# Performance work log

Hardware: AMD Instinct MI355X
Metric: run time of the kernel (lower is better)

## Reference

```python
import jax, jax.numpy as jnp
import numpy as np

A, B_HI = 0.0, 1.0          # support interval
NUM_GRIDS = 256
DEGREE = 2
KNOTS = (0.33, 0.66)
NUM_BASIS = DEGREE + 1 + len(KNOTS)  # 5


def spline_basis(d):
    # Truncated power basis: [1, d, d^2, relu(d-k1)^2, relu(d-k2)^2] -> [B, NUM_BASIS]
    cols = [jnp.ones_like(d)]
    for p in range(1, DEGREE + 1):
        cols.append(d ** p)
    for k in KNOTS:
        cols.append(jax.nn.relu(d - k) ** DEGREE)
    return jnp.stack(cols, axis=1)


def setup_inputs() -> dict:
    key = jax.random.key(0)
    k1, k2, k3, k4 = jax.random.split(key, 4)
    B, IN = 65536, 128
    OUT = NUM_GRIDS + 1
    d = jax.random.uniform(k1, (B,), dtype=jnp.float32)          # treatment in [0,1]
    z = jax.random.normal(k2, (B, IN), dtype=jnp.float32)        # encoder features
    weight = jax.random.uniform(k3, (IN, OUT, NUM_BASIS), dtype=jnp.float32)  # torch.rand init
    bias = jax.random.uniform(k4, (OUT, NUM_BASIS), dtype=jnp.float32)
    return {"d": d, "z": z, "weight": weight, "bias": bias}


def reference(d, z, weight, bias):
    basis = spline_basis(d)  # [B, NB]
    # einsum('ab,bcd->acd') then sum over basis dim, fused into one contraction
    out = jnp.einsum('bi,ion,bn->bo', z, weight, basis) + basis @ bias.T  # [B, OUT]
    # linear interpolation params (faithful to get_linear_interpolation_params,
    # including tmp = (d - a) * (b - a))
    tmp = (d - A) * (B_HI - A)
    g = tmp * NUM_GRIDS
    lower = jnp.clip(jnp.floor(g), 0, NUM_GRIDS - 1)
    upper = jnp.clip(jnp.ceil(g), 0, NUM_GRIDS - 1)
    dist = g - lower
    li = lower.astype(jnp.int32)
    ui = upper.astype(jnp.int32)
    ix = jnp.arange(out.shape[0])
    lb = out[ix, li]
    ub = out[ix, ui]
    prob = lb + (ub - lb) * dist
    in_support = (d >= A) & (d <= B_HI)
    return prob * in_support.astype(prob.dtype)
```

## Files before the change

### kernel.cpp

```cpp
#include <hip/hip_runtime.h>
#include <math.h>


constexpr int IN_F = 128;
constexpr int OUTC = 257;
constexpr int NB   = 5;

__global__ __launch_bounds__(256) void transpose_w_kernel(
    const float* __restrict__ w, float* __restrict__ wT)
{
    int idx = blockIdx.x * blockDim.x + threadIdx.x;
    constexpr int TOT = OUTC * NB * IN_F;
    if (idx >= TOT) return;
    int i    = idx & (IN_F - 1);
    int rest = idx >> 7;
    int n    = rest % NB;
    int o    = rest / NB;
    wT[idx] = w[(size_t)i * (OUTC * NB) + o * NB + n];
}

template<bool TR>
__global__ __launch_bounds__(256) void vcd_main(
    const float* __restrict__ dtr, const float* __restrict__ z,
    const float* __restrict__ w,   const float* __restrict__ bias,
    float* __restrict__ out, int B)
{
    int t   = blockIdx.x * blockDim.x + threadIdx.x;
    int row = t >> 4;
    int s   = threadIdx.x & 15;
    if (row >= B) return;

    float dv = dtr[row];

    float b1 = dv, b2 = dv * dv;
    float r1 = fmaxf(dv - 0.33f, 0.0f);
    float r2 = fmaxf(dv - 0.66f, 0.0f);
    float b3 = r1 * r1, b4 = r2 * r2;

    float g     = dv * 256.0f;
    float lower = fminf(fmaxf(floorf(g), 0.0f), 255.0f);
    float dist  = g - lower;
    int   li = (int)lower;
    int   ui = min(li + 1, 255);

    const float4* zv = reinterpret_cast<const float4*>(z + (size_t)row * IN_F + s * 8);
    float4 z0 = zv[0], z1 = zv[1];
    float zz[8] = {z0.x, z0.y, z0.z, z0.w, z1.x, z1.y, z1.z, z1.w};

    float accl = 0.0f, accu = 0.0f;

    if constexpr (TR) {
        const float* wl = w + (size_t)li * (NB * IN_F) + s * 8;
        const float* wu = w + (size_t)ui * (NB * IN_F) + s * 8;
        #pragma unroll
        for (int n = 0; n < NB; ++n) {
            float bn = (n == 0) ? 1.0f : (n == 1) ? b1 : (n == 2) ? b2 : (n == 3) ? b3 : b4;
            float4 l0 = reinterpret_cast<const float4*>(wl + n * IN_F)[0];
            float4 l1 = reinterpret_cast<const float4*>(wl + n * IN_F)[1];
            float4 u0 = reinterpret_cast<const float4*>(wu + n * IN_F)[0];
            float4 u1 = reinterpret_cast<const float4*>(wu + n * IN_F)[1];
            float dl = zz[0]*l0.x + zz[1]*l0.y + zz[2]*l0.z + zz[3]*l0.w
                     + zz[4]*l1.x + zz[5]*l1.y + zz[6]*l1.z + zz[7]*l1.w;
            float du = zz[0]*u0.x + zz[1]*u0.y + zz[2]*u0.z + zz[3]*u0.w
                     + zz[4]*u1.x + zz[5]*u1.y + zz[6]*u1.z + zz[7]*u1.w;
            accl = fmaf(bn, dl, accl);
            accu = fmaf(bn, du, accu);
        }
    } else {
        #pragma unroll
        for (int k = 0; k < 8; ++k) {
            const float* wp  = w + (size_t)(s * 8 + k) * (OUTC * NB);
            const float* wlp = wp + li * NB;
            const float* wup = wp + ui * NB;
            float wsl = wlp[0] + b1*wlp[1] + b2*wlp[2] + b3*wlp[3] + b4*wlp[4];
            float wsu = wup[0] + b1*wup[1] + b2*wup[2] + b3*wup[3] + b4*wup[4];
            accl = fmaf(zz[k], wsl, accl);
            accu = fmaf(zz[k], wsu, accu);
        }
    }

    float comb = fmaf(dist, accu - accl, accl);
    #pragma unroll
    for (int m = 1; m < 16; m <<= 1)
        comb += __shfl_xor(comb, m, 64);

    if (s == 0) {
        const float* blp = bias + li * NB;
        const float* bup = bias + ui * NB;
        float bl = blp[0] + b1*blp[1] + b2*blp[2] + b3*blp[3] + b4*blp[4];
        float bu = bup[0] + b1*bup[1] + b2*bup[2] + b3*bup[3] + b4*bup[4];
        float prob = comb + fmaf(dist, bu - bl, bl);
        bool sup = (dv >= 0.0f) && (dv <= 1.0f);
        out[row] = sup ? prob : 0.0f;
    }
}

extern "C" void kernel_launch(void* const* d_in, const int* in_sizes, int n_in,
                              void* d_out, int out_size, void* d_ws, size_t ws_size,
                              hipStream_t stream) {
    const float* d_d = (const float*)d_in[0];
    const float* d_z = (const float*)d_in[1];
    const float* d_w = (const float*)d_in[2];
    const float* d_b = (const float*)d_in[3];
    float* out = (float*)d_out;
    int B = in_sizes[0];

    constexpr size_t WT_BYTES = (size_t)OUTC * NB * IN_F * sizeof(float);
    int main_blocks = (B * 16 + 255) / 256;

    if (ws_size >= WT_BYTES) {
        float* wT = (float*)d_ws;
        constexpr int TOT = OUTC * NB * IN_F;
        transpose_w_kernel<<<(TOT + 255) / 256, 256, 0, stream>>>(d_w, wT);
        vcd_main<true><<<main_blocks, 256, 0, stream>>>(d_d, d_z, wT, d_b, out, B);
    } else {
        vcd_main<false><<<main_blocks, 256, 0, stream>>>(d_d, d_z, d_w, d_b, out, B);
    }
}
```

Measured before the change: 103.3 us.

## Bucket rows by grid cell and stage cell weights in LDS

Rows are bucketed by their lower grid index using atomic counters into a per-cell order list. A per-cell kernel then loads the two relevant weight slices and biases into shared memory once and processes all rows of that cell, replacing scattered per-row global weight gathers. Rows that overflow a bucket's capacity fall back to a serial per-thread dot product in the scatter kernel. The change adds an extra launch, atomics and an indirect z gather, and block counts are fixed at cells times split regardless of how many rows each cell holds.

```diff
diff --git a/kernel.cpp b/kernel.cpp
--- a/kernel.cpp
+++ b/kernel.cpp
@@ -2,95 +2,184 @@
 #include <math.h>
 
 
-constexpr int IN_F = 128;
-constexpr int OUTC = 257;
-constexpr int NB   = 5;
-
-__global__ __launch_bounds__(256) void transpose_w_kernel(
-    const float* __restrict__ w, float* __restrict__ wT)
-{
-    int idx = blockIdx.x * blockDim.x + threadIdx.x;
+constexpr int IN_F  = 128;
+constexpr int OUTC  = 257;
+constexpr int NB    = 5;
+constexpr int CELLS = 256;
+constexpr int CAP   = 1024;
+constexpr int SPLIT = 8;
+
+constexpr size_t ORDER_OFF = 4096;
+constexpr size_t WT_OFF    = ORDER_OFF + (size_t)CELLS * CAP * 4;
+constexpr size_t WS_NEED   = WT_OFF + (size_t)OUTC * NB * IN_F * 4;
+
+__global__ __launch_bounds__(256) void init_kernel(
+    const float* __restrict__ w, float* __restrict__ wT, int* __restrict__ cursor)
+{
+    int idx = blockIdx.x * 256 + threadIdx.x;
+    if (idx < CELLS) cursor[idx] = 0;
     constexpr int TOT = OUTC * NB * IN_F;
-    if (idx >= TOT) return;
-    int i    = idx & (IN_F - 1);
-    int rest = idx >> 7;
-    int n    = rest % NB;
-    int o    = rest / NB;
-    wT[idx] = w[(size_t)i * (OUTC * NB) + o * NB + n];
-}
-
-template<bool TR>
-__global__ __launch_bounds__(256) void vcd_main(
+    if (idx < TOT) {
+        int i    = idx & (IN_F - 1);
+        int rest = idx >> 7;
+        int n    = rest % NB;
+        int o    = rest / NB;
+        wT[idx] = w[(size_t)i * (OUTC * NB) + o * NB + n];
+    }
+}
+
+__global__ __launch_bounds__(256) void scatter_kernel(
+    const float* __restrict__ dtr, const float* __restrict__ z,
+    const float* __restrict__ wT,  const float* __restrict__ bias,
+    int* __restrict__ cursor, int* __restrict__ order,
+    float* __restrict__ out, int B)
+{
+    int row = blockIdx.x * 256 + threadIdx.x;
+    if (row >= B) return;
+    float dv = dtr[row];
+    float g  = dv * 256.0f;
+    int li   = (int)fminf(fmaxf(floorf(g), 0.0f), 255.0f);
+    int slot = atomicAdd(&cursor[li], 1);
+    if (slot < CAP) { order[li * CAP + slot] = row; return; }
+
+    int   ui   = min(li + 1, 255);
+    float dist = g - (float)li;
+    float b1 = dv, b2 = dv * dv;
+    float r1 = fmaxf(dv - 0.33f, 0.0f), r2 = fmaxf(dv - 0.66f, 0.0f);
+    float bas[NB] = {1.0f, b1, b2, r1 * r1, r2 * r2};
+    const float* wl = wT + (size_t)li * (NB * IN_F);
+    const float* wu = wT + (size_t)ui * (NB * IN_F);
+    const float* zr = z + (size_t)row * IN_F;
+    float accl = 0.0f, accu = 0.0f;
+    for (int n = 0; n < NB; ++n) {
+        float sl = 0.0f, su = 0.0f;
+        for (int i = 0; i < IN_F; ++i) {
+            sl = fmaf(zr[i], wl[n * IN_F + i], sl);
+            su = fmaf(zr[i], wu[n * IN_F + i], su);
+        }
+        accl = fmaf(bas[n], sl, accl);
+        accu = fmaf(bas[n], su, accu);
+    }
+    float bl = 0.0f, bu = 0.0f;
+    for (int n = 0; n < NB; ++n) {
+        bl = fmaf(bas[n], bias[li * NB + n], bl);
+        bu = fmaf(bas[n], bias[ui * NB + n], bu);
+    }
+    float lb = accl + bl, ub = accu + bu;
+    float prob = lb + (ub - lb) * dist;
+    bool  sup  = (dv >= 0.0f) && (dv <= 1.0f);
+    out[row] = sup ? prob : 0.0f;
+}
+
+__global__ __launch_bounds__(256) void main_kernel(
+    const float* __restrict__ dtr, const float* __restrict__ z,
+    const float* __restrict__ wT,  const float* __restrict__ bias,
+    const int* __restrict__ cursor, const int* __restrict__ order,
+    float* __restrict__ out)
+{
+    __shared__ float lds[2 * NB * IN_F + 2 * NB + 6];
+    int c = blockIdx.x / SPLIT;
+    int s = blockIdx.x % SPLIT;
+    int u = min(c + 1, 255);
+    int tid = threadIdx.x;
+
+    const float4* wl4 = reinterpret_cast<const float4*>(wT + (size_t)c * (NB * IN_F));
+    const float4* wu4 = reinterpret_cast<const float4*>(wT + (size_t)u * (NB * IN_F));
+    float4* l4 = reinterpret_cast<float4*>(lds);
+    for (int k = tid; k < 320; k += 256)
+        l4[k] = (k < 160) ? wl4[k] : wu4[k - 160];
+    if (tid < NB)            lds[1280 + tid] = bias[c * NB + tid];
+    else if (tid < 2 * NB)   lds[1280 + tid] = bias[u * NB + tid - NB];
+    __syncthreads();
+
+    int cnt  = min(cursor[c], CAP);
+    int grp  = tid >> 4;
+    int lane = tid & 15;
+
+    for (int j = s * 16 + grp; j < cnt; j += SPLIT * 16) {
+        int   row = order[c * CAP + j];
+        float dv  = dtr[row];
+        float b1 = dv, b2 = dv * dv;
+        float r1 = fmaxf(dv - 0.33f, 0.0f), r2 = fmaxf(dv - 0.66f, 0.0f);
+        float b3 = r1 * r1, b4 = r2 * r2;
+        float dist = dv * 256.0f - (float)c;
+
+        const float4* zv = reinterpret_cast<const float4*>(z + (size_t)row * IN_F + lane * 8);
+        float4 z0 = zv[0], z1 = zv[1];
+
+        float accl = 0.0f, accu = 0.0f;
+        #pragma unroll
+        for (int n = 0; n < NB; ++n) {
+            float bn = (n == 0) ? 1.0f : (n == 1) ? b1 : (n == 2) ? b2 : (n == 3) ? b3 : b4;
+            const float4* ln4 = reinterpret_cast<const float4*>(lds + n * IN_F);
+            const float4* un4 = reinterpret_cast<const float4*>(lds + NB * IN_F + n * IN_F);
+            float4 l0 = ln4[lane * 2], l1 = ln4[lane * 2 + 1];
+            float4 u0 = un4[lane * 2], u1 = un4[lane * 2 + 1];
+            float dl = z0.x*l0.x + z0.y*l0.y + z0.z*l0.z + z0.w*l0.w
+                     + z1.x*l1.x + z1.y*l1.y + z1.z*l1.z + z1.w*l1.w;
+            float du = z0.x*u0.x + z0.y*u0.y + z0.z*u0.z + z0.w*u0.w
+                     + z1.x*u1.x + z1.y*u1.y + z1.z*u1.z + z1.w*u1.w;
+            accl = fmaf(bn, dl, accl);
+            accu = fmaf(bn, du, accu);
+        }
+
+        float comb = fmaf(dist, accu - accl, accl);
+        #pragma unroll
+        for (int m = 1; m < 16; m <<= 1)
+            comb += __shfl_xor(comb, m, 64);
+
+        if (lane == 0) {
+            float bl = lds[1280] + b1*lds[1281] + b2*lds[1282] + b3*lds[1283] + b4*lds[1284];
+            float bu = lds[1285] + b1*lds[1286] + b2*lds[1287] + b3*lds[1288] + b4*lds[1289];
+            float prob = comb + fmaf(dist, bu - bl, bl);
+            bool  sup  = (dv >= 0.0f) && (dv <= 1.0f);
+            out[row] = sup ? prob : 0.0f;
+        }
+    }
+}
+
+__global__ __launch_bounds__(256) void direct_kernel(
     const float* __restrict__ dtr, const float* __restrict__ z,
     const float* __restrict__ w,   const float* __restrict__ bias,
     float* __restrict__ out, int B)
 {
     int t   = blockIdx.x * blockDim.x + threadIdx.x;
     int row = t >> 4;
-    int s   = threadIdx.x & 15;
+    int lane = threadIdx.x & 15;
     if (row >= B) return;
-
     float dv = dtr[row];
-
     float b1 = dv, b2 = dv * dv;
-    float r1 = fmaxf(dv - 0.33f, 0.0f);
-    float r2 = fmaxf(dv - 0.66f, 0.0f);
+    float r1 = fmaxf(dv - 0.33f, 0.0f), r2 = fmaxf(dv - 0.66f, 0.0f);
     float b3 = r1 * r1, b4 = r2 * r2;
-
-    float g     = dv * 256.0f;
+    float g = dv * 256.0f;
     float lower = fminf(fmaxf(floorf(g), 0.0f), 255.0f);
-    float dist  = g - lower;
-    int   li = (int)lower;
-    int   ui = min(li + 1, 255);
-
-    const float4* zv = reinterpret_cast<const float4*>(z + (size_t)row * IN_F + s * 8);
+    float dist = g - lower;
+    int li = (int)lower, ui = min(li + 1, 255);
+    const float4* zv = reinterpret_cast<const float4*>(z + (size_t)row * IN_F + lane * 8);
     float4 z0 = zv[0], z1 = zv[1];
     float zz[8] = {z0.x, z0.y, z0.z, z0.w, z1.x, z1.y, z1.z, z1.w};
-
     float accl = 0.0f, accu = 0.0f;
-
-    if constexpr (TR) {
-        const float* wl = w + (size_t)li * (NB * IN_F) + s * 8;
-        const float* wu = w + (size_t)ui * (NB * IN_F) + s * 8;
-        #pragma unroll
-        for (int n = 0; n < NB; ++n) {
-            float bn = (n == 0) ? 1.0f : (n == 1) ? b1 : (n == 2) ? b2 : (n == 3) ? b3 : b4;
-            float4 l0 = reinterpret_cast<const float4*>(wl + n * IN_F)[0];
-            float4 l1 = reinterpret_cast<const float4*>(wl + n * IN_F)[1];
-            float4 u0 = reinterpret_cast<const float4*>(wu + n * IN_F)[0];
-            float4 u1 = reinterpret_cast<const float4*>(wu + n * IN_F)[1];
-            float dl = zz[0]*l0.x + zz[1]*l0.y + zz[2]*l0.z + zz[3]*l0.w
-                     + zz[4]*l1.x + zz[5]*l1.y + zz[6]*l1.z + zz[7]*l1.w;
-            float du = zz[0]*u0.x + zz[1]*u0.y + zz[2]*u0.z + zz[3]*u0.w
-                     + zz[4]*u1.x + zz[5]*u1.y + zz[6]*u1.z + zz[7]*u1.w;
-            accl = fmaf(bn, dl, accl);
-            accu = fmaf(bn, du, accu);
-        }
-    } else {
-        #pragma unroll
-        for (int k = 0; k < 8; ++k) {
-            const float* wp  = w + (size_t)(s * 8 + k) * (OUTC * NB);
-            const float* wlp = wp + li * NB;
-            const float* wup = wp + ui * NB;
-            float wsl = wlp[0] + b1*wlp[1] + b2*wlp[2] + b3*wlp[3] + b4*wlp[4];
-            float wsu = wup[0] + b1*wup[1] + b2*wup[2] + b3*wup[3] + b4*wup[4];
-            accl = fmaf(zz[k], wsl, accl);
-            accu = fmaf(zz[k], wsu, accu);
-        }
-    }
-
+    #pragma unroll
+    for (int k = 0; k < 8; ++k) {
+        const float* wp  = w + (size_t)(lane * 8 + k) * (OUTC * NB);
+        const float* wlp = wp + li * NB;
+        const float* wup = wp + ui * NB;
+        float wsl = wlp[0] + b1*wlp[1] + b2*wlp[2] + b3*wlp[3] + b4*wlp[4];
+        float wsu = wup[0] + b1*wup[1] + b2*wup[2] + b3*wup[3] + b4*wup[4];
+        accl = fmaf(zz[k], wsl, accl);
+        accu = fmaf(zz[k], wsu, accu);
+    }
     float comb = fmaf(dist, accu - accl, accl);
     #pragma unroll
     for (int m = 1; m < 16; m <<= 1)
         comb += __shfl_xor(comb, m, 64);
-
-    if (s == 0) {
+    if (lane == 0) {
         const float* blp = bias + li * NB;
         const float* bup = bias + ui * NB;
         float bl = blp[0] + b1*blp[1] + b2*blp[2] + b3*blp[3] + b4*blp[4];
         float bu = bup[0] + b1*bup[1] + b2*bup[2] + b3*bup[3] + b4*bup[4];
         float prob = comb + fmaf(dist, bu - bl, bl);
-        bool sup = (dv >= 0.0f) && (dv <= 1.0f);
+        bool  sup  = (dv >= 0.0f) && (dv <= 1.0f);
         out[row] = sup ? prob : 0.0f;
     }
 }
@@ -105,15 +194,17 @@
     float* out = (float*)d_out;
     int B = in_sizes[0];
 
-    constexpr size_t WT_BYTES = (size_t)OUTC * NB * IN_F * sizeof(float);
-    int main_blocks = (B * 16 + 255) / 256;
-
-    if (ws_size >= WT_BYTES) {
-        float* wT = (float*)d_ws;
-        constexpr int TOT = OUTC * NB * IN_F;
-        transpose_w_kernel<<<(TOT + 255) / 256, 256, 0, stream>>>(d_w, wT);
-        vcd_main<true><<<main_blocks, 256, 0, stream>>>(d_d, d_z, wT, d_b, out, B);
-    } else {
-        vcd_main<false><<<main_blocks, 256, 0, stream>>>(d_d, d_z, d_w, d_b, out, B);
-    }
-}
+    if (ws_size < WS_NEED) {
+        direct_kernel<<<(B * 16 + 255) / 256, 256, 0, stream>>>(d_d, d_z, d_w, d_b, out, B);
+        return;
+    }
+
+    int*   cursor = (int*)d_ws;
+    int*   order  = (int*)((char*)d_ws + ORDER_OFF);
+    float* wT     = (float*)((char*)d_ws + WT_OFF);
+
+    constexpr int TOT = OUTC * NB * IN_F;
+    init_kernel<<<(TOT + 255) / 256, 256, 0, stream>>>(d_w, wT, cursor);
+    scatter_kernel<<<(B + 255) / 256, 256, 0, stream>>>(d_d, d_z, wT, d_b, cursor, order, out, B);
+    main_kernel<<<CELLS * SPLIT, 256, 0, stream>>>(d_d, d_z, wT, d_b, cursor, order, out);
+}
```

After: 121.8 us. 1.18x slower.

## Precompute per-interval quadratic coefficients folding knot terms into polynomial basis

Applied to the files above, without the earlier changes.

Replaces the weight transpose with a coefficient kernel that expands the truncated-power basis into plain quadratic coefficients per grid cell, with two extra sub-intervals for the cells containing the knots. Each row then loads 6 coefficient vectors instead of 10 weight vectors and evaluates the lower and upper quadratics by Horner's rule. The aim is to cut weight traffic and FMAs per row in the main kernel. The knot-cell selection relies on the float comparison against 0.33 and 0.66 matching the relu branch, which could introduce small rounding differences.

```diff
diff --git a/kernel.cpp b/kernel.cpp
--- a/kernel.cpp
+++ b/kernel.cpp
@@ -4,93 +4,142 @@
 
 constexpr int IN_F = 128;
 constexpr int OUTC = 257;
-constexpr int NB   = 5;
+constexpr int NSUB = 258;
+constexpr size_t A_FLOATS  = (size_t)NSUB * 6 * IN_F;
+constexpr size_t BQ_OFF_F  = A_FLOATS;
+constexpr size_t WS_NEED   = (A_FLOATS + NSUB * 6) * sizeof(float);
 
-__global__ __launch_bounds__(256) void transpose_w_kernel(
-    const float* __restrict__ w, float* __restrict__ wT)
+__global__ __launch_bounds__(256) void coeff_kernel(
+    const float* __restrict__ w, const float* __restrict__ bias,
+    float* __restrict__ A, float* __restrict__ Bq)
 {
-    int idx = blockIdx.x * blockDim.x + threadIdx.x;
-    constexpr int TOT = OUTC * NB * IN_F;
-    if (idx >= TOT) return;
-    int i    = idx & (IN_F - 1);
-    int rest = idx >> 7;
-    int n    = rest % NB;
-    int o    = rest / NB;
-    wT[idx] = w[(size_t)i * (OUTC * NB) + o * NB + n];
+    int t = blockIdx.x * 256 + threadIdx.x;
+    if (t >= NSUB * IN_F) return;
+    int i   = t & (IN_F - 1);
+    int idx = t >> 7;
+    int c   = (idx < 256) ? idx : (idx == 256 ? 84 : 168);
+    int u   = min(c + 1, 255);
+    float s1 = ((c >= 85) || (idx == 256)) ? 1.0f : 0.0f;
+    float s2 = ((c >= 169) || (idx == 257)) ? 1.0f : 0.0f;
+    const float k1 = 0.33f, k2 = 0.66f;
+
+    const float* wl = w + (size_t)i * (OUTC * 5) + c * 5;
+    const float* wu = w + (size_t)i * (OUTC * 5) + u * 5;
+    float q0l = wl[0] + s1 * k1 * k1 * wl[3] + s2 * k2 * k2 * wl[4];
+    float q1l = wl[1] - 2.0f * (s1 * k1 * wl[3] + s2 * k2 * wl[4]);
+    float q2l = wl[2] + s1 * wl[3] + s2 * wl[4];
+    float q0u = wu[0] + s1 * k1 * k1 * wu[3] + s2 * k2 * k2 * wu[4];
+    float q1u = wu[1] - 2.0f * (s1 * k1 * wu[3] + s2 * k2 * wu[4]);
+    float q2u = wu[2] + s1 * wu[3] + s2 * wu[4];
+
+    float* Ai = A + (size_t)idx * (6 * IN_F);
+    Ai[0 * IN_F + i] = q0l;  Ai[1 * IN_F + i] = q1l;  Ai[2 * IN_F + i] = q2l;
+    Ai[3 * IN_F + i] = q0u;  Ai[4 * IN_F + i] = q1u;  Ai[5 * IN_F + i] = q2u;
+
+    if (i == 0) {
+        const float* bl = bias + c * 5;
+        const float* bu = bias + u * 5;
+        float* bq = Bq + idx * 6;
+        bq[0] = bl[0] + s1 * k1 * k1 * bl[3] + s2 * k2 * k2 * bl[4];
+        bq[1] = bl[1] - 2.0f * (s1 * k1 * bl[3] + s2 * k2 * bl[4]);
+        bq[2] = bl[2] + s1 * bl[3] + s2 * bl[4];
+        bq[3] = bu[0] + s1 * k1 * k1 * bu[3] + s2 * k2 * k2 * bu[4];
+        bq[4] = bu[1] - 2.0f * (s1 * k1 * bu[3] + s2 * k2 * bu[4]);
+        bq[5] = bu[2] + s1 * bu[3] + s2 * bu[4];
+    }
 }
 
-template<bool TR>
-__global__ __launch_bounds__(256) void vcd_main(
+__global__ __launch_bounds__(256) void eval_kernel(
+    const float* __restrict__ dtr, const float* __restrict__ z,
+    const float* __restrict__ A,   const float* __restrict__ Bq,
+    float* __restrict__ out, int B)
+{
+    int t   = blockIdx.x * 256 + threadIdx.x;
+    int row = t >> 4;
+    int s   = threadIdx.x & 15;
+    if (row >= B) return;
+
+    float dv = dtr[row];
+    float g  = dv * 256.0f;
+    float lower = fminf(fmaxf(floorf(g), 0.0f), 255.0f);
+    int   c  = (int)lower;
+    float x  = g - lower;
+    int  idx = c;
+    if      (c ==  84 && dv >= 0.33f) idx = 256;
+    else if (c == 168 && dv >= 0.66f) idx = 257;
+
+    const float4* zv = reinterpret_cast<const float4*>(z + (size_t)row * IN_F + s * 8);
+    float4 z0 = zv[0], z1 = zv[1];
+
+    const float* Ai = A + (size_t)idx * (6 * IN_F) + s * 8;
+    float D[6];
+    #pragma unroll
+    for (int p = 0; p < 6; ++p) {
+        const float4* ap = reinterpret_cast<const float4*>(Ai + p * IN_F);
+        float4 a0 = ap[0], a1 = ap[1];
+        D[p] = z0.x*a0.x + z0.y*a0.y + z0.z*a0.z + z0.w*a0.w
+             + z1.x*a1.x + z1.y*a1.y + z1.z*a1.z + z1.w*a1.w;
+    }
+    float Pl = (D[2] * dv + D[1]) * dv + D[0];
+    float Pu = (D[5] * dv + D[4]) * dv + D[3];
+    float val = Pl + x * (Pu - Pl);
+
+    #pragma unroll
+    for (int m = 1; m < 16; m <<= 1)
+        val += __shfl_xor(val, m, 64);
+
+    if (s == 0) {
+        const float* bq = Bq + idx * 6;
+        float Bl = (bq[2] * dv + bq[1]) * dv + bq[0];
+        float Bu = (bq[5] * dv + bq[4]) * dv + bq[3];
+        val += Bl + x * (Bu - Bl);
+        bool sup = (dv >= 0.0f) && (dv <= 1.0f);
+        out[row] = sup ? val : 0.0f;
+    }
+}
+
+__global__ __launch_bounds__(256) void direct_kernel(
     const float* __restrict__ dtr, const float* __restrict__ z,
     const float* __restrict__ w,   const float* __restrict__ bias,
     float* __restrict__ out, int B)
 {
     int t   = blockIdx.x * blockDim.x + threadIdx.x;
     int row = t >> 4;
-    int s   = threadIdx.x & 15;
+    int lane = threadIdx.x & 15;
     if (row >= B) return;
-
     float dv = dtr[row];
-
     float b1 = dv, b2 = dv * dv;
-    float r1 = fmaxf(dv - 0.33f, 0.0f);
-    float r2 = fmaxf(dv - 0.66f, 0.0f);
+    float r1 = fmaxf(dv - 0.33f, 0.0f), r2 = fmaxf(dv - 0.66f, 0.0f);
     float b3 = r1 * r1, b4 = r2 * r2;
-
-    float g     = dv * 256.0f;
+    float g = dv * 256.0f;
     float lower = fminf(fmaxf(floorf(g), 0.0f), 255.0f);
-    float dist  = g - lower;
-    int   li = (int)lower;
-    int   ui = min(li + 1, 255);
-
-    const float4* zv = reinterpret_cast<const float4*>(z + (size_t)row * IN_F + s * 8);
+    float dist = g - lower;
+    int li = (int)lower, ui = min(li + 1, 255);
+    const float4* zv = reinterpret_cast<const float4*>(z + (size_t)row * IN_F + lane * 8);
     float4 z0 = zv[0], z1 = zv[1];
     float zz[8] = {z0.x, z0.y, z0.z, z0.w, z1.x, z1.y, z1.z, z1.w};
-
     float accl = 0.0f, accu = 0.0f;
-
-    if constexpr (TR) {
-        const float* wl = w + (size_t)li * (NB * IN_F) + s * 8;
-        const float* wu = w + (size_t)ui * (NB * IN_F) + s * 8;
-        #pragma unroll
-        for (int n = 0; n < NB; ++n) {
-            float bn = (n == 0) ? 1.0f : (n == 1) ? b1 : (n == 2) ? b2 : (n == 3) ? b3 : b4;
-            float4 l0 = reinterpret_cast<const float4*>(wl + n * IN_F)[0];
-            float4 l1 = reinterpret_cast<const float4*>(wl + n * IN_F)[1];
-            float4 u0 = reinterpret_cast<const float4*>(wu + n * IN_F)[0];
-            float4 u1 = reinterpret_cast<const float4*>(wu + n * IN_F)[1];
-            float dl = zz[0]*l0.x + zz[1]*l0.y + zz[2]*l0.z + zz[3]*l0.w
-                     + zz[4]*l1.x + zz[5]*l1.y + zz[6]*l1.z + zz[7]*l1.w;
-            float du = zz[0]*u0.x + zz[1]*u0.y + zz[2]*u0.z + zz[3]*u0.w
-                     + zz[4]*u1.x + zz[5]*u1.y + zz[6]*u1.z + zz[7]*u1.w;
-            accl = fmaf(bn, dl, accl);
-            accu = fmaf(bn, du, accu);
-        }
-    } else {
-        #pragma unroll
-        for (int k = 0; k < 8; ++k) {
-            const float* wp  = w + (size_t)(s * 8 + k) * (OUTC * NB);
-            const float* wlp = wp + li * NB;
-            const float* wup = wp + ui * NB;
-            float wsl = wlp[0] + b1*wlp[1] + b2*wlp[2] + b3*wlp[3] + b4*wlp[4];
-            float wsu = wup[0] + b1*wup[1] + b2*wup[2] + b3*wup[3] + b4*wup[4];
-            accl = fmaf(zz[k], wsl, accl);
-            accu = fmaf(zz[k], wsu, accu);
-        }
+    #pragma unroll
+    for (int k = 0; k < 8; ++k) {
+        const float* wp  = w + (size_t)(lane * 8 + k) * (OUTC * 5);
+        const float* wlp = wp + li * 5;
+        const float* wup = wp + ui * 5;
+        float wsl = wlp[0] + b1*wlp[1] + b2*wlp[2] + b3*wlp[3] + b4*wlp[4];
+        float wsu = wup[0] + b1*wup[1] + b2*wup[2] + b3*wup[3] + b4*wup[4];
+        accl = fmaf(zz[k], wsl, accl);
+        accu = fmaf(zz[k], wsu, accu);
     }
-
     float comb = fmaf(dist, accu - accl, accl);
     #pragma unroll
     for (int m = 1; m < 16; m <<= 1)
         comb += __shfl_xor(comb, m, 64);
-
-    if (s == 0) {
-        const float* blp = bias + li * NB;
-        const float* bup = bias + ui * NB;
+    if (lane == 0) {
+        const float* blp = bias + li * 5;
+        const float* bup = bias + ui * 5;
         float bl = blp[0] + b1*blp[1] + b2*blp[2] + b3*blp[3] + b4*blp[4];
         float bu = bup[0] + b1*bup[1] + b2*bup[2] + b3*bup[3] + b4*bup[4];
         float prob = comb + fmaf(dist, bu - bl, bl);
-        bool sup = (dv >= 0.0f) && (dv <= 1.0f);
+        bool  sup  = (dv >= 0.0f) && (dv <= 1.0f);
         out[row] = sup ? prob : 0.0f;
     }
 }
@@ -105,15 +154,15 @@
     float* out = (float*)d_out;
     int B = in_sizes[0];
 
-    constexpr size_t WT_BYTES = (size_t)OUTC * NB * IN_F * sizeof(float);
-    int main_blocks = (B * 16 + 255) / 256;
+    if (ws_size < WS_NEED) {
+        direct_kernel<<<(B * 16 + 255) / 256, 256, 0, stream>>>(d_d, d_z, d_w, d_b, out, B);
+        return;
+    }
 
-    if (ws_size >= WT_BYTES) {
-        float* wT = (float*)d_ws;
-        constexpr int TOT = OUTC * NB * IN_F;
-        transpose_w_kernel<<<(TOT + 255) / 256, 256, 0, stream>>>(d_w, wT);
-        vcd_main<true><<<main_blocks, 256, 0, stream>>>(d_d, d_z, wT, d_b, out, B);
-    } else {
-        vcd_main<false><<<main_blocks, 256, 0, stream>>>(d_d, d_z, d_w, d_b, out, B);
-    }
+    float* A  = (float*)d_ws;
+    float* Bq = (float*)d_ws + BQ_OFF_F;
+
+    constexpr int CT = NSUB * IN_F;
+    coeff_kernel<<<(CT + 255) / 256, 256, 0, stream>>>(d_w, d_b, A, Bq);
+    eval_kernel<<<(B * 16 + 255) / 256, 256, 0, stream>>>(d_d, d_z, A, Bq, out, B);
 }
```

Measured after the change: 91.38 us. 11.5% less time.
